# Kernel tuning notes

Measured on AMD Instinct MI355X. Metric: run time of the kernel, lower is better.

The kernel has to match this reference:

```python
import jax, jax.numpy as jnp
import numpy as np

B = 128          # graphs
NPG = 512        # nodes per graph
N = B * NPG      # total nodes
DEG = 8
E = N * DEG      # total edges (intra-graph)
D = 100          # num_feature_dim / num_node_labels
HID = 128        # config.hidden
HEADS = 8
F1 = 20          # per-head dim of first GATConv in each GATNet
RATIO = 0.5
K = int(np.ceil(RATIO * NPG))  # nodes kept per graph by SAGPooling
NEG_SLOPE = 0.2


def setup_inputs() -> dict:
    key = jax.random.key(0)
    ks = jax.random.split(key, 24)
    x = jax.random.randint(ks[0], (N,), 0, D)
    # intra-graph random edges: local ids in [0, NPG) + graph offset
    src_l = jax.random.randint(ks[1], (B, NPG * DEG), 0, NPG)
    dst_l = jax.random.randint(ks[2], (B, NPG * DEG), 0, NPG)
    off = (jnp.arange(B) * NPG)[:, None]
    edge_index = jnp.stack([(src_l + off).ravel(), (dst_l + off).ravel()])
    batch = jnp.repeat(jnp.arange(B), NPG)

    def lin(k, fan_in, fan_out):
        return jax.random.normal(k, (fan_in, fan_out), jnp.float32) / np.sqrt(fan_in)

    def att(k, h, f):
        return jax.random.normal(k, (h, f), jnp.float32) * 0.1

    p = {
        # GATNet A (conv1): GATConv(D, 20, heads=8) then GATConv(160, HID, heads=1)
        "W_a1": lin(ks[3], D, HEADS * F1), "asrc_a1": att(ks[4], HEADS, F1),
        "adst_a1": att(ks[5], HEADS, F1), "b_a1": jnp.zeros((HEADS * F1,), jnp.float32),
        "W_a2": lin(ks[6], HEADS * F1, HID), "asrc_a2": att(ks[7], 1, HID),
        "adst_a2": att(ks[8], 1, HID), "b_a2": jnp.zeros((HID,), jnp.float32),
        # GATNet B (conv4): GATConv(HID, 20, heads=8) then GATConv(160, HID, heads=1)
        "W_b1": lin(ks[9], HID, HEADS * F1), "asrc_b1": att(ks[10], HEADS, F1),
        "adst_b1": att(ks[11], HEADS, F1), "b_b1": jnp.zeros((HEADS * F1,), jnp.float32),
        "W_b2": lin(ks[12], HEADS * F1, HID), "asrc_b2": att(ks[13], 1, HID),
        "adst_b2": att(ks[14], 1, HID), "b_b2": jnp.zeros((HID,), jnp.float32),
        # SAGPooling GraphConv(HID, 1)
        "w_rel": lin(ks[15], HID, 1), "w_root": lin(ks[16], HID, 1),
        "b_pool": jnp.zeros((1,), jnp.float32),
    }
    return {"x": x, "edge_index": edge_index, "batch": batch, **p}


def _gat_conv(h, src, dst, W, asrc, adst, b):
    """PyG GATConv (with self-loops already included in src/dst)."""
    Hh, Ff = asrc.shape
    z = (h @ W).reshape(N, Hh, Ff)                       # [N,H,F]
    es = jnp.sum(z * asrc, axis=-1)                      # [N,H] source logits
    ed = jnp.sum(z * adst, axis=-1)                      # [N,H] dest logits
    e = jax.nn.leaky_relu(es[src] + ed[dst], NEG_SLOPE)  # [E',H]
    m = jax.ops.segment_max(e, dst, num_segments=N)
    m = jnp.where(jnp.isfinite(m), m, 0.0)
    ex = jnp.exp(e - m[dst])
    den = jax.ops.segment_sum(ex, dst, num_segments=N)
    alpha = ex / (den[dst] + 1e-16)
    out = jax.ops.segment_sum(z[src] * alpha[:, :, None], dst, num_segments=N)
    return out.reshape(N, Hh * Ff) + b


def reference(x, edge_index, batch,
              W_a1, asrc_a1, adst_a1, b_a1, W_a2, asrc_a2, adst_a2, b_a2,
              W_b1, asrc_b1, adst_b1, b_b1, W_b2, asrc_b2, adst_b2, b_b2,
              w_rel, w_root, b_pool):
    src, dst = edge_index[0], edge_index[1]
    loops = jnp.arange(N)
    src_sl = jnp.concatenate([src, loops])  # GATConv adds self loops
    dst_sl = jnp.concatenate([dst, loops])

    h = jax.nn.one_hot(x, D, dtype=jnp.float32)
    # GATNet A: conv1 -> relu -> conv2 ; outer relu (dropout is eval no-op)
    h = jax.nn.relu(_gat_conv(h, src_sl, dst_sl, W_a1, asrc_a1, adst_a1, b_a1))
    h = _gat_conv(h, src_sl, dst_sl, W_a2, asrc_a2, adst_a2, b_a2)
    h = jax.nn.relu(h)
    # GATNet B
    h = jax.nn.relu(_gat_conv(h, src_sl, dst_sl, W_b1, asrc_b1, adst_b1, b_b1))
    h = _gat_conv(h, src_sl, dst_sl, W_b2, asrc_b2, adst_b2, b_b2)
    h = jax.nn.relu(h)

    # SAGPooling: GraphConv(HID,1) score (no self loops), tanh, per-graph top-k
    nbr = jax.ops.segment_sum(h[src], dst, num_segments=N)
    score = jnp.tanh(nbr @ w_rel + h @ w_root + b_pool).ravel()   # [N]
    sv, si = jax.lax.top_k(score.reshape(B, NPG), K)              # [B,K]
    perm = (si + (jnp.arange(B) * NPG)[:, None]).ravel()          # global node ids
    x_sel = h[perm] * sv.ravel()[:, None]                         # [B*K, HID]
    pooled = jnp.max(x_sel.reshape(B, K, HID), axis=1)            # global_max_pool
    batch_out = jnp.repeat(jnp.arange(B), K)
    return (pooled, perm, sv.ravel(), batch_out)
```

## Files before the change

### kernel.cpp

```cpp
#include <hip/hip_runtime.h>
#include <math.h>

#define N_NODES 65536
#define NPG     512
#define NGRAPH  128
#define E_EDGES 524288
#define MAXDEG  64
#define NHEADS  8
#define F1      20
#define HID     128
#define D160    160
#define KSEL    256
#define NLBL    100

#define IMG_A2_ELEMS (144*168)
#define IMG_B1_ELEMS (176*136)
#define PB_ZERO 0
#define PB_A2   64
#define PB_B1   (PB_A2 + 95)
#define PB_B2   (PB_B1 + 94)
#define PB_WA1  (PB_B2 + 95)
#define PB_EST  (PB_WA1 + 63)
#define PB_TOT  (PB_EST + 7)

typedef unsigned short ushort_t;
typedef unsigned int   uint_t;
typedef unsigned long long u64;
typedef __attribute__((ext_vector_type(8))) short short8;
typedef __attribute__((ext_vector_type(4))) float f32x4;

__device__ __forceinline__ float lrelu(float x){ return x > 0.f ? x : 0.2f*x; }
__device__ __forceinline__ ushort_t f2bf(float f){
    uint_t u = __float_as_uint(f);
    return (ushort_t)((u + 0x7FFFu + ((u >> 16) & 1u)) >> 16);
}
__device__ __forceinline__ float bf2f(ushort_t u){ return __uint_as_float(((uint_t)u) << 16); }
__device__ __forceinline__ float bflo(uint_t v){ return __uint_as_float(v << 16); }
__device__ __forceinline__ float bfhi(uint_t v){ return __uint_as_float(v & 0xFFFF0000u); }
__device__ __forceinline__ int xswz(int bid, int nblocks){
    return (bid & 7) * (nblocks >> 3) + (bid >> 3);
}
__device__ __forceinline__ float rdlanef(float v, int i){
    return __uint_as_float((uint_t)__builtin_amdgcn_readlane(__float_as_int(v), i));
}

__device__ __forceinline__ u64 comp_make(float s, int idx){
    uint_t u = __float_as_uint(s);
    u ^= (u & 0x80000000u) ? 0xFFFFFFFFu : 0x80000000u;
    return ((u64)u << 32) | (u64)(511 - idx);
}
__device__ __forceinline__ float comp_score(u64 c){
    uint_t u = (uint_t)(c >> 32);
    u ^= (u & 0x80000000u) ? 0x80000000u : 0xFFFFFFFFu;
    return __uint_as_float(u);
}
__device__ __forceinline__ int comp_idx(u64 c){ return 511 - (int)(c & 0x1FFu); }
__device__ __forceinline__ u64 shfl_xor_u64(u64 x, int m){
    uint_t lo = __shfl_xor((uint_t)x, m);
    uint_t hi = __shfl_xor((uint_t)(x >> 32), m);
    return ((u64)hi << 32) | lo;
}

__global__ void k_prep(const float* __restrict__ Wa1, const float* __restrict__ as1,
                       const float* __restrict__ ad1,
                       const float* __restrict__ Wa2, const float* __restrict__ as2,
                       const float* __restrict__ ad2,
                       const float* __restrict__ Wb1, const float* __restrict__ asb1,
                       const float* __restrict__ adb1,
                       const float* __restrict__ Wb2, const float* __restrict__ asb2,
                       const float* __restrict__ adb2,
                       int* __restrict__ deg,
                       ushort_t* __restrict__ imgA2, ushort_t* __restrict__ imgB1,
                       ushort_t* __restrict__ imgB2,
                       ushort_t* __restrict__ Wbf, float* __restrict__ esT,
                       float* __restrict__ edT){
    int bid = blockIdx.x, tid = threadIdx.x;
    if(bid < PB_A2){
        ((uint4*)deg)[(bid - PB_ZERO)*256 + tid] = (uint4){0,0,0,0};
    } else if(bid < PB_B1 || (bid >= PB_B2 && bid < PB_WA1)){
        bool isB2 = (bid >= PB_B2);
        int j = (bid - (isB2 ? PB_B2 : PB_A2))*256 + tid;
        if(j < IMG_A2_ELEMS){
            const float* W  = isB2 ? Wb2 : Wa2;
            const float* as = isB2 ? asb2 : as2;
            const float* ad = isB2 ? adb2 : ad2;
            int n = j / 168, k = j - n*168;
            float v = 0.f;
            if(k < 160){
                if(n < 128) v = W[k*128 + n];
                else if(n < 130){
                    const float* av = (n == 128) ? as : ad;
                    float s = 0.f;
                    for(int c=0; c<128; ++c) s += W[k*128 + c]*av[c];
                    v = s;
                }
            }
            (isB2 ? imgB2 : imgA2)[j] = f2bf(v);
        }
    } else if(bid < PB_B2){
        int j = (bid - PB_B1)*256 + tid;
        if(j < IMG_B1_ELEMS){
            int n = j / 136, k = j - n*136;
            float v = 0.f;
            if(k < 128){
                if(n < 160) v = Wb1[k*160 + n];
                else {
                    int j2 = n - 160, h = j2 & 7;
                    const float* av = ((j2 < 8) ? asb1 : adb1) + h*F1;
                    const float* wr = Wb1 + k*160 + h*F1;
                    float s = 0.f;
                    #pragma unroll
                    for(int f=0; f<F1; ++f) s += wr[f]*av[f];
                    v = s;
                }
            }
            imgB1[j] = f2bf(v);
        }
    } else if(bid < PB_EST){
        int j = (bid - PB_WA1)*256 + tid;
        if(j < NLBL*D160) Wbf[j] = f2bf(Wa1[j]);
    } else {
        int t = (bid - PB_EST)*256 + tid;
        if(t < NLBL*16){
            int lbl = t >> 4, j = t & 15, h = j & 7;
            const float* av = ((j < 8) ? as1 : ad1) + h*F1;
            const float* wr = Wa1 + lbl*D160 + h*F1;
            float s = 0.f;
            #pragma unroll
            for(int f=0; f<F1; ++f) s += wr[f]*av[f];
            if(j < 8) esT[lbl*8 + h] = s;
            else      edT[lbl*8 + h] = s;
        }
    }
}

__global__ void k_build_ell(const int* __restrict__ src, const int* __restrict__ dst,
                            int* __restrict__ deg, int* __restrict__ ell){
    int blk = xswz(blockIdx.x, E_EDGES/256);
    int e = blk*blockDim.x + threadIdx.x;
    int d = dst[e];
    int p = atomicAdd(&deg[d], 1);
    if(p < MAXDEG) ell[d*MAXDEG + p] = src[e];
}

__global__ __launch_bounds__(256) void k_attn8_a(const int* __restrict__ x,
        const int* __restrict__ deg, const int* __restrict__ ell,
        const ushort_t* __restrict__ Wbf, const float* __restrict__ esT,
        const float* __restrict__ edT, const float* __restrict__ bias,
        ushort_t* __restrict__ out){
    __shared__ __align__(16) ushort_t Wl[NLBL*D160];
    __shared__ float esL[NLBL*8], edL[NLBL*8];
    int tid = threadIdx.x;
    for(int i = tid; i < NLBL*D160/8; i += 256)
        ((uint4*)Wl)[i] = ((const uint4*)Wbf)[i];
    for(int i = tid; i < NLBL*8; i += 256){ esL[i] = esT[i]; edL[i] = edT[i]; }
    __syncthreads();
    int blk = xswz(blockIdx.x, N_NODES*NHEADS/256);
    int t = blk*256 + tid;
    int n = t >> 3, h = t & 7;
    int dg = deg[n]; if(dg > MAXDEG) dg = MAXDEG;
    int lbl = x[n];
    float edn = edL[lbl*8 + h];
    float wself = expf(lrelu(esL[lbl*8 + h] + edn));
    float den = wself;
    float acc[F1];
    {
        const uint_t* zn = (const uint_t*)Wl + lbl*80 + h*10;
        #pragma unroll
        for(int f=0; f<10; ++f){
            uint_t v = zn[f];
            acc[2*f]   = wself*bflo(v);
            acc[2*f+1] = wself*bfhi(v);
        }
    }
    const int* el = ell + n*MAXDEG;
    int i = 0;
    for(; i+2 <= dg; i += 2){
        int sa = el[i], sb = el[i+1];
        int la = x[sa], lb = x[sb];
        float wa = expf(lrelu(esL[la*8 + h] + edn));
        float wb = expf(lrelu(esL[lb*8 + h] + edn));
        den += wa + wb;
        const uint_t* za = (const uint_t*)Wl + la*80 + h*10;
        const uint_t* zb = (const uint_t*)Wl + lb*80 + h*10;
        #pragma unroll
        for(int f=0; f<10; ++f){
            uint_t va = za[f], vb = zb[f];
            acc[2*f]   += wa*bflo(va) + wb*bflo(vb);
            acc[2*f+1] += wa*bfhi(va) + wb*bfhi(vb);
        }
    }
    if(i < dg){
        int sa = el[i];
        int la = x[sa];
        float wa = expf(lrelu(esL[la*8 + h] + edn));
        den += wa;
        const uint_t* za = (const uint_t*)Wl + la*80 + h*10;
        #pragma unroll
        for(int f=0; f<10; ++f){
            uint_t va = za[f];
            acc[2*f]   += wa*bflo(va);
            acc[2*f+1] += wa*bfhi(va);
        }
    }
    float inv = 1.f/(den + 1e-16f);
    uint_t* o = (uint_t*)(out + (size_t)n*D160 + h*F1);
    const float* bb = bias + h*F1;
    #pragma unroll
    for(int f=0; f<10; ++f){
        float v0 = fmaxf(acc[2*f]*inv   + bb[2*f],   0.f);
        float v1 = fmaxf(acc[2*f+1]*inv + bb[2*f+1], 0.f);
        o[f] = (uint_t)f2bf(v0) | ((uint_t)f2bf(v1) << 16);
    }
}

__global__ __launch_bounds__(512) void k_attn8b(const int* __restrict__ deg,
        const int* __restrict__ ell, const ushort_t* __restrict__ z8,
        const float* __restrict__ es8, const float* __restrict__ ed8,
        const float* __restrict__ bias, ushort_t* __restrict__ out){
    __shared__ __align__(16) ushort_t zl[512*88];
    __shared__ __align__(16) float4 esl[512];
    __shared__ __align__(16) float4 edl[512];
    int tid = threadIdx.x;
    int blk = xswz(blockIdx.x, NGRAPH*2);
    int g = blk >> 1, hg = blk & 1;
    int base = g*NPG;
    for(int idx = tid; idx < 512*10; idx += 512){
        int row = idx/10, q = idx - (idx/10)*10;
        uint4 v = *(const uint4*)(z8 + (size_t)(base+row)*D160 + hg*80 + q*8);
        *(uint4*)(zl + row*88 + q*8) = v;
    }
    esl[tid] = *(const float4*)(es8 + (size_t)(base+tid)*8 + hg*4);
    edl[tid] = *(const float4*)(ed8 + (size_t)(base+tid)*8 + hg*4);
    __syncthreads();
    int n = tid;
    int dg = deg[base+n]; if(dg > MAXDEG) dg = MAXDEG;
    const int* el = ell + (size_t)(base+n)*MAXDEG;
    float4 edn = edl[n];
    float4 esn = esl[n];
    float w0 = expf(lrelu(esn.x + edn.x));
    float w1 = expf(lrelu(esn.y + edn.y));
    float w2 = expf(lrelu(esn.z + edn.z));
    float w3 = expf(lrelu(esn.w + edn.w));
    float den0 = w0, den1 = w1, den2 = w2, den3 = w3;
    float acc[80];
    #pragma unroll
    for(int q=0; q<10; ++q){
        uint4 v = *(const uint4*)(zl + n*88 + q*8);
        const uint_t* vu = (const uint_t*)&v;
        #pragma unroll
        for(int r=0; r<4; ++r){
            int ch = q*8 + r*2;
            float wA = (ch < 20) ? w0 : (ch < 40) ? w1 : (ch < 60) ? w2 : w3;
            float wB = (ch+1 < 20) ? w0 : (ch+1 < 40) ? w1 : (ch+1 < 60) ? w2 : w3;
            acc[ch]   = wA*bflo(vu[r]);
            acc[ch+1] = wB*bfhi(vu[r]);
        }
    }
    for(int i=0; i<dg; ++i){
        int s = el[i] & (NPG-1);
        float4 es_s = esl[s];
        float wa0 = expf(lrelu(es_s.x + edn.x));
        float wa1 = expf(lrelu(es_s.y + edn.y));
        float wa2 = expf(lrelu(es_s.z + edn.z));
        float wa3 = expf(lrelu(es_s.w + edn.w));
        den0 += wa0; den1 += wa1; den2 += wa2; den3 += wa3;
        #pragma unroll
        for(int q=0; q<10; ++q){
            uint4 v = *(const uint4*)(zl + s*88 + q*8);
            const uint_t* vu = (const uint_t*)&v;
            #pragma unroll
            for(int r=0; r<4; ++r){
                int ch = q*8 + r*2;
                float wA = (ch < 20) ? wa0 : (ch < 40) ? wa1 : (ch < 60) ? wa2 : wa3;
                float wB = (ch+1 < 20) ? wa0 : (ch+1 < 40) ? wa1 : (ch+1 < 60) ? wa2 : wa3;
                acc[ch]   += wA*bflo(vu[r]);
                acc[ch+1] += wB*bfhi(vu[r]);
            }
        }
    }
    float inv0 = 1.f/(den0 + 1e-16f);
    float inv1 = 1.f/(den1 + 1e-16f);
    float inv2 = 1.f/(den2 + 1e-16f);
    float inv3 = 1.f/(den3 + 1e-16f);
    const float* bb = bias + hg*80;
    uint_t* o = (uint_t*)out + (size_t)(base+n)*80 + hg*40;
    #pragma unroll
    for(int q=0; q<10; ++q){
        #pragma unroll
        for(int r=0; r<4; ++r){
            int ch = q*8 + r*2;
            float iA = (ch < 20) ? inv0 : (ch < 40) ? inv1 : (ch < 60) ? inv2 : inv3;
            float iB = (ch+1 < 20) ? inv0 : (ch+1 < 40) ? inv1 : (ch+1 < 60) ? inv2 : inv3;
            float v0 = fmaxf(acc[ch]*iA   + bb[ch],   0.f);
            float v1 = fmaxf(acc[ch+1]*iB + bb[ch+1], 0.f);
            o[q*4 + r] = (uint_t)f2bf(v0) | ((uint_t)f2bf(v1) << 16);
        }
    }
}

template<int IN, int OUTC, int OUTIMG, bool ESED8>
__global__ __launch_bounds__(256) void k_gemm2(const ushort_t* __restrict__ Wimg,
                                               const ushort_t* __restrict__ A,
                                               ushort_t* __restrict__ C,
                                               float* __restrict__ oa,
                                               float* __restrict__ ob){
    constexpr int LDW = IN + 8;
    constexpr int NT = OUTIMG/16;
    constexpr int NC = OUTC/16;
    constexpr int KS = IN/32;
    constexpr int ELEMS = OUTIMG*LDW;
    __shared__ __align__(16) ushort_t Wt[ELEMS];
    int tid = threadIdx.x;
    int blk = xswz(blockIdx.x, N_NODES/64);
    int wave = tid >> 6, lane = tid & 63;
    int col16 = lane & 15;
    int kq = (lane >> 4) * 8;
    int row = blk*64 + wave*16 + col16;
    const ushort_t* Ar = A + (size_t)row*IN + kq;
    short8 afr[KS];
    #pragma unroll
    for(int ks=0; ks<KS; ++ks)
        afr[ks] = *reinterpret_cast<const short8*>(Ar + ks*32);
    for(int i = tid; i < ELEMS/8; i += 256)
        ((uint4*)Wt)[i] = ((const uint4*)Wimg)[i];
    __syncthreads();
    f32x4 acc[NT];
    #pragma unroll
    for(int c=0;c<NT;++c) acc[c] = (f32x4){0.f,0.f,0.f,0.f};
    #pragma unroll
    for(int ks=0; ks<KS; ++ks){
        #pragma unroll
        for(int c=0;c<NT;++c){
            short8 bf = *reinterpret_cast<const short8*>(&Wt[(c*16 + col16)*LDW + ks*32 + kq]);
            acc[c] = __builtin_amdgcn_mfma_f32_16x16x32_bf16(afr[ks], bf, acc[c], 0, 0, 0);
        }
    }
    int rbase = blk*64 + wave*16 + (lane >> 4)*4;
    #pragma unroll
    for(int c=0;c<NC;++c){
        #pragma unroll
        for(int r=0;r<4;++r){
            C[(size_t)(rbase + r)*OUTC + c*16 + col16] = f2bf(acc[c][r]);
        }
    }
    if(ESED8){
        #pragma unroll
        for(int r=0;r<4;++r){
            float v = acc[NT-1][r];
            if(col16 < 8) oa[(size_t)(rbase + r)*8 + col16] = v;
            else          ob[(size_t)(rbase + r)*8 + (col16 - 8)] = v;
        }
    } else {
        if(col16 == 0){
            #pragma unroll
            for(int r=0;r<4;++r) oa[rbase + r] = acc[NT-1][r];
        }
        if(col16 == 1){
            #pragma unroll
            for(int r=0;r<4;++r) ob[rbase + r] = acc[NT-1][r];
        }
    }
}

template<typename OutT, bool DOT>
__global__ void k_attn1(const int* __restrict__ deg, const int* __restrict__ ell,
                        const ushort_t* __restrict__ Z, const float* __restrict__ es,
                        const float* __restrict__ ed, const float* __restrict__ bias,
                        OutT* __restrict__ out,
                        const float* __restrict__ wa, const float* __restrict__ wb,
                        float* __restrict__ oa, float* __restrict__ ob){
    int blk = xswz(blockIdx.x, N_NODES/4);
    int gt = blk*blockDim.x + threadIdx.x;
    int n = gt >> 6;
    int l = threadIdx.x & 63;
    int dg = deg[n]; if(dg > MAXDEG) dg = MAXDEG;
    float edn = ed[n];
    float wself = expf(lrelu(es[n] + edn));
    int s_l = 0; float w_l = 0.f;
    if(l < dg){ s_l = ell[n*MAXDEG + l]; w_l = expf(lrelu(es[s_l] + edn)); }
    float den = w_l;
    for(int o=32;o>0;o>>=1) den += __shfl_xor(den,o);
    den += wself;
    const uint_t* Zu = (const uint_t*)Z;
    uint_t zn = Zu[(size_t)n*64 + l];
    float acc0 = wself*bflo(zn);
    float acc1 = wself*bfhi(zn);
    int i = 0;
    for(; i+4 <= dg; i += 4){
        int s0 = __builtin_amdgcn_readlane(s_l, i);
        int s1 = __builtin_amdgcn_readlane(s_l, i+1);
        int s2 = __builtin_amdgcn_readlane(s_l, i+2);
        int s3 = __builtin_amdgcn_readlane(s_l, i+3);
        uint_t z0 = Zu[(size_t)s0*64 + l];
        uint_t z1 = Zu[(size_t)s1*64 + l];
        uint_t z2 = Zu[(size_t)s2*64 + l];
        uint_t z3 = Zu[(size_t)s3*64 + l];
        float w0 = rdlanef(w_l, i);
        float w1 = rdlanef(w_l, i+1);
        float w2 = rdlanef(w_l, i+2);
        float w3 = rdlanef(w_l, i+3);
        acc0 += w0*bflo(z0) + w1*bflo(z1);
        acc1 += w0*bfhi(z0) + w1*bfhi(z1);
        acc0 += w2*bflo(z2) + w3*bflo(z3);
        acc1 += w2*bfhi(z2) + w3*bfhi(z3);
    }
    for(; i < dg; ++i){
        int s0 = __builtin_amdgcn_readlane(s_l, i);
        float w0 = rdlanef(w_l, i);
        uint_t z0 = Zu[(size_t)s0*64 + l];
        acc0 += w0*bflo(z0);
        acc1 += w0*bfhi(z0);
    }
    float inv = 1.f/(den + 1e-16f);
    float2 bb = ((const float2*)bias)[l];
    float r0 = fmaxf(acc0*inv + bb.x, 0.f);
    float r1 = fmaxf(acc1*inv + bb.y, 0.f);
    if(sizeof(OutT) == 2){
        ((uint_t*)out)[(size_t)n*64 + l] = (uint_t)f2bf(r0) | ((uint_t)f2bf(r1) << 16);
    } else {
        float2 rv; rv.x = r0; rv.y = r1;
        ((float2*)out)[(size_t)n*64 + l] = rv;
    }
    if(DOT){
        float2 a2 = ((const float2*)wa)[l];
        float2 b2 = ((const float2*)wb)[l];
        float pa = r0*a2.x + r1*a2.y;
        float pb = r0*b2.x + r1*b2.y;
        for(int o=32;o>0;o>>=1){ pa += __shfl_xor(pa,o); pb += __shfl_xor(pb,o); }
        if(l==0){ oa[n] = pa; ob[n] = pb; }
    }
}

__global__ void k_score(const int* __restrict__ deg, const int* __restrict__ ell,
                        const float* __restrict__ yrel, const float* __restrict__ rroot,
                        const float* __restrict__ bpool, float* __restrict__ score){
    int blk = xswz(blockIdx.x, N_NODES/256);
    int n = blk*blockDim.x + threadIdx.x;
    int dg = deg[n]; if(dg > MAXDEG) dg = MAXDEG;
    float s = rroot[n] + bpool[0];
    const int* el = ell + n*MAXDEG;
    int i = 0;
    for(; i+4 <= dg; i += 4){
        float y0 = yrel[el[i]],   y1 = yrel[el[i+1]];
        float y2 = yrel[el[i+2]], y3 = yrel[el[i+3]];
        s += (y0 + y1) + (y2 + y3);
    }
    for(; i < dg; ++i) s += yrel[el[i]];
    score[n] = tanhf(s);
}

__global__ __launch_bounds__(512) void k_topk_pool(const float* __restrict__ score,
                                                   const ushort_t* __restrict__ H,
                                                   float* __restrict__ pooled,
                                                   float* __restrict__ perm_f,
                                                   float* __restrict__ sv,
                                                   float* __restrict__ batch_f){
    __shared__ int   sidx[KSEL];
    __shared__ float sval[KSEL];
    __shared__ float pmax[512];
    int g = xswz(blockIdx.x, NGRAPH);
    int base = g*NPG;
    int t = threadIdx.x;
    if(t < 64){
        int l = t;
        u64 v[8];
        #pragma unroll
        for(int r=0;r<8;++r){
            int i = r*64 + l;
            v[r] = comp_make(score[base + i], i);
        }
        #pragma unroll
        for(int kk=1; kk<=9; ++kk){
            int k = 1 << kk;
            #pragma unroll
            for(int jj=kk-1; jj>=0; --jj){
                int j = 1 << jj;
                if(j < 64){
                    bool lower = (l & j) == 0;
                    #pragma unroll
                    for(int r=0;r<8;++r){
                        int i = r*64 + l;
                        u64 p = shfl_xor_u64(v[r], j);
                        bool desc = (i & k) == 0;
                        u64 mx = v[r] > p ? v[r] : p;
                        u64 mn = v[r] > p ? p : v[r];
                        v[r] = (lower == desc) ? mx : mn;
                    }
                } else {
                    int jr = j >> 6;
                    #pragma unroll
                    for(int r=0;r<8;++r){
                        if((r & jr) == 0){
                            int rp = r | jr;
                            int i = r*64 + l;
                            bool desc = (i & k) == 0;
                            u64 a = v[r], b = v[rp];
                            u64 mx = a > b ? a : b;
                            u64 mn = a > b ? b : a;
                            v[r]  = desc ? mx : mn;
                            v[rp] = desc ? mn : mx;
                        }
                    }
                }
            }
        }
        #pragma unroll
        for(int r=0;r<4;++r){
            int i = r*64 + l;
            int idx = comp_idx(v[r]);
            float s = comp_score(v[r]);
            perm_f[g*KSEL + i]  = (float)(base + idx);
            sv[g*KSEL + i]      = s;
            batch_f[g*KSEL + i] = (float)g;
            sidx[i] = idx; sval[i] = s;
        }
    }
    __syncthreads();
    int c = t & 127, kc = t >> 7;
    float mx = -1e30f;
    for(int kk = kc*64; kk < kc*64 + 64; ++kk){
        mx = fmaxf(mx, bf2f(H[(size_t)(base + sidx[kk])*HID + c]) * sval[kk]);
    }
    pmax[t] = mx;
    __syncthreads();
    if(t < HID){
        pooled[g*HID + t] = fmaxf(fmaxf(pmax[t], pmax[t+128]),
                                  fmaxf(pmax[t+256], pmax[t+384]));
    }
}

extern "C" void kernel_launch(void* const* d_in, const int* in_sizes, int n_in,
                              void* d_out, int out_size, void* d_ws, size_t ws_size,
                              hipStream_t stream) {
    const int*   x       = (const int*)  d_in[0];
    const int*   eidx    = (const int*)  d_in[1];
    const float* W_a1    = (const float*)d_in[3];
    const float* asrc_a1 = (const float*)d_in[4];
    const float* adst_a1 = (const float*)d_in[5];
    const float* b_a1    = (const float*)d_in[6];
    const float* W_a2    = (const float*)d_in[7];
    const float* asrc_a2 = (const float*)d_in[8];
    const float* adst_a2 = (const float*)d_in[9];
    const float* b_a2    = (const float*)d_in[10];
    const float* W_b1    = (const float*)d_in[11];
    const float* asrc_b1 = (const float*)d_in[12];
    const float* adst_b1 = (const float*)d_in[13];
    const float* b_b1    = (const float*)d_in[14];
    const float* W_b2    = (const float*)d_in[15];
    const float* asrc_b2 = (const float*)d_in[16];
    const float* adst_b2 = (const float*)d_in[17];
    const float* b_b2    = (const float*)d_in[18];
    const float* w_rel   = (const float*)d_in[19];
    const float* w_root  = (const float*)d_in[20];
    const float* b_pool  = (const float*)d_in[21];

    const int* e_src = eidx;
    const int* e_dst = eidx + E_EDGES;

    char* ws = (char*)d_ws;
    size_t off = 0;
    auto alloc = [&](size_t bytes)->char*{
        char* p = ws + off;
        off += (bytes + 255) & ~(size_t)255;
        return p;
    };
    int*      deg    = (int*)     alloc((size_t)N_NODES*4);
    int*      ell    = (int*)     alloc((size_t)N_NODES*MAXDEG*4);
    ushort_t* z8     = (ushort_t*)alloc((size_t)N_NODES*D160*2);
    ushort_t* h8     = (ushort_t*)alloc((size_t)N_NODES*D160*2);
    ushort_t* zc     = (ushort_t*)alloc((size_t)N_NODES*HID*2);
    ushort_t* hmid   = (ushort_t*)alloc((size_t)N_NODES*HID*2);
    ushort_t* hfin   = (ushort_t*)alloc((size_t)N_NODES*HID*2);
    float*    es8    = (float*)   alloc((size_t)N_NODES*NHEADS*4);
    float*    ed8    = (float*)   alloc((size_t)N_NODES*NHEADS*4);
    float*    es1    = (float*)   alloc((size_t)N_NODES*4);
    float*    ed1    = (float*)   alloc((size_t)N_NODES*4);
    float*    yrel   = (float*)   alloc((size_t)N_NODES*4);
    float*    rroot  = (float*)   alloc((size_t)N_NODES*4);
    float*    score  = (float*)   alloc((size_t)N_NODES*4);
    ushort_t* Wbf    = (ushort_t*)alloc((size_t)NLBL*D160*2);
    float*    esT    = (float*)   alloc((size_t)NLBL*8*4);
    float*    edT    = (float*)   alloc((size_t)NLBL*8*4);
    ushort_t* imgA2  = (ushort_t*)alloc((size_t)IMG_A2_ELEMS*2);
    ushort_t* imgB1  = (ushort_t*)alloc((size_t)IMG_B1_ELEMS*2);
    ushort_t* imgB2  = (ushort_t*)alloc((size_t)IMG_A2_ELEMS*2);
    (void)ws_size; (void)n_in; (void)in_sizes; (void)out_size;

    float* out      = (float*)d_out;
    float* pooled   = out;
    float* perm_f   = out + NGRAPH*HID;
    float* sv       = perm_f + NGRAPH*KSEL;
    float* batch_f  = sv + NGRAPH*KSEL;

    k_prep<<<PB_TOT, 256, 0, stream>>>(W_a1, asrc_a1, adst_a1,
                                       W_a2, asrc_a2, adst_a2,
                                       W_b1, asrc_b1, adst_b1,
                                       W_b2, asrc_b2, adst_b2,
                                       deg, imgA2, imgB1, imgB2, Wbf, esT, edT);
    k_build_ell<<<E_EDGES/256, 256, 0, stream>>>(e_src, e_dst, deg, ell);

    k_attn8_a<<<N_NODES*NHEADS/256, 256, 0, stream>>>(x, deg, ell, Wbf, esT, edT, b_a1, h8);

    k_gemm2<D160, HID, 144, false><<<N_NODES/64, 256, 0, stream>>>(imgA2, h8, zc, es1, ed1);
    k_attn1<ushort_t, false><<<N_NODES/4, 256, 0, stream>>>(deg, ell, zc, es1, ed1, b_a2, hmid,
                                                            nullptr, nullptr, nullptr, nullptr);

    k_gemm2<HID, D160, 176, true><<<N_NODES/64, 256, 0, stream>>>(imgB1, hmid, z8, es8, ed8);
    k_attn8b<<<NGRAPH*2, 512, 0, stream>>>(deg, ell, z8, es8, ed8, b_b1, h8);

    k_gemm2<D160, HID, 144, false><<<N_NODES/64, 256, 0, stream>>>(imgB2, h8, zc, es1, ed1);
    k_attn1<ushort_t, true><<<N_NODES/4, 256, 0, stream>>>(deg, ell, zc, es1, ed1, b_b2, hfin,
                                                           w_rel, w_root, yrel, rroot);

    k_score<<<N_NODES/256, 256, 0, stream>>>(deg, ell, yrel, rroot, b_pool, score);
    k_topk_pool<<<NGRAPH, NPG, 0, stream>>>(score, hfin, pooled, perm_f, sv, batch_f);
}
```

Baseline: 226.2 us.

## Rework single-head GAT aggregation to four threads per node with vector loads

Result: no change. 226.5 us (+0.1%).

```diff
diff --git a/kernel.cpp b/kernel.cpp
--- a/kernel.cpp
+++ b/kernel.cpp
@@ -39,9 +39,6 @@
 __device__ __forceinline__ float bfhi(uint_t v){ return __uint_as_float(v & 0xFFFF0000u); }
 __device__ __forceinline__ int xswz(int bid, int nblocks){
     return (bid & 7) * (nblocks >> 3) + (bid >> 3);
-}
-__device__ __forceinline__ float rdlanef(float v, int i){
-    return __uint_as_float((uint_t)__builtin_amdgcn_readlane(__float_as_int(v), i));
 }
 
 __device__ __forceinline__ u64 comp_make(float s, int idx){
@@ -363,72 +360,105 @@
     }
 }
 
-template<typename OutT, bool DOT>
-__global__ void k_attn1(const int* __restrict__ deg, const int* __restrict__ ell,
-                        const ushort_t* __restrict__ Z, const float* __restrict__ es,
-                        const float* __restrict__ ed, const float* __restrict__ bias,
-                        OutT* __restrict__ out,
-                        const float* __restrict__ wa, const float* __restrict__ wb,
-                        float* __restrict__ oa, float* __restrict__ ob){
-    int blk = xswz(blockIdx.x, N_NODES/4);
-    int gt = blk*blockDim.x + threadIdx.x;
-    int n = gt >> 6;
-    int l = threadIdx.x & 63;
+template<bool DOT>
+__global__ void k_attn1v(const int* __restrict__ deg, const int* __restrict__ ell,
+                         const ushort_t* __restrict__ Z, const float* __restrict__ es,
+                         const float* __restrict__ ed, const float* __restrict__ bias,
+                         ushort_t* __restrict__ out,
+                         const float* __restrict__ wa, const float* __restrict__ wb,
+                         float* __restrict__ oa, float* __restrict__ ob){
+    int blk = xswz(blockIdx.x, N_NODES*4/256);
+    int t = blk*256 + threadIdx.x;
+    int n = t >> 2, qt = t & 3;
     int dg = deg[n]; if(dg > MAXDEG) dg = MAXDEG;
     float edn = ed[n];
     float wself = expf(lrelu(es[n] + edn));
-    int s_l = 0; float w_l = 0.f;
-    if(l < dg){ s_l = ell[n*MAXDEG + l]; w_l = expf(lrelu(es[s_l] + edn)); }
-    float den = w_l;
-    for(int o=32;o>0;o>>=1) den += __shfl_xor(den,o);
-    den += wself;
-    const uint_t* Zu = (const uint_t*)Z;
-    uint_t zn = Zu[(size_t)n*64 + l];
-    float acc0 = wself*bflo(zn);
-    float acc1 = wself*bfhi(zn);
+    float den = wself;
+    const uint4* Zu = (const uint4*)Z;
+    float acc[32];
+    {
+        const uint4* zr = Zu + (size_t)n*16 + qt*4;
+        uint4 vs[4];
+        #pragma unroll
+        for(int q=0;q<4;++q) vs[q] = zr[q];
+        #pragma unroll
+        for(int q=0;q<4;++q){
+            const uint_t* vu = (const uint_t*)&vs[q];
+            #pragma unroll
+            for(int r=0;r<4;++r){
+                acc[q*8+r*2]   = wself*bflo(vu[r]);
+                acc[q*8+r*2+1] = wself*bfhi(vu[r]);
+            }
+        }
+    }
+    const int* el = ell + (size_t)n*MAXDEG;
     int i = 0;
-    for(; i+4 <= dg; i += 4){
-        int s0 = __builtin_amdgcn_readlane(s_l, i);
-        int s1 = __builtin_amdgcn_readlane(s_l, i+1);
-        int s2 = __builtin_amdgcn_readlane(s_l, i+2);
-        int s3 = __builtin_amdgcn_readlane(s_l, i+3);
-        uint_t z0 = Zu[(size_t)s0*64 + l];
-        uint_t z1 = Zu[(size_t)s1*64 + l];
-        uint_t z2 = Zu[(size_t)s2*64 + l];
-        uint_t z3 = Zu[(size_t)s3*64 + l];
-        float w0 = rdlanef(w_l, i);
-        float w1 = rdlanef(w_l, i+1);
-        float w2 = rdlanef(w_l, i+2);
-        float w3 = rdlanef(w_l, i+3);
-        acc0 += w0*bflo(z0) + w1*bflo(z1);
-        acc1 += w0*bfhi(z0) + w1*bfhi(z1);
-        acc0 += w2*bflo(z2) + w3*bflo(z3);
-        acc1 += w2*bfhi(z2) + w3*bfhi(z3);
-    }
-    for(; i < dg; ++i){
-        int s0 = __builtin_amdgcn_readlane(s_l, i);
-        float w0 = rdlanef(w_l, i);
-        uint_t z0 = Zu[(size_t)s0*64 + l];
-        acc0 += w0*bflo(z0);
-        acc1 += w0*bfhi(z0);
+    for(; i+2 <= dg; i += 2){
+        int sa = el[i], sb = el[i+1];
+        float ea = es[sa], eb = es[sb];
+        const uint4* za = Zu + (size_t)sa*16 + qt*4;
+        const uint4* zb = Zu + (size_t)sb*16 + qt*4;
+        uint4 va[4], vb4[4];
+        #pragma unroll
+        for(int q=0;q<4;++q){ va[q] = za[q]; vb4[q] = zb[q]; }
+        float wA = expf(lrelu(ea + edn));
+        float wB = expf(lrelu(eb + edn));
+        den += wA + wB;
+        #pragma unroll
+        for(int q=0;q<4;++q){
+            const uint_t* au = (const uint_t*)&va[q];
+            const uint_t* bu = (const uint_t*)&vb4[q];
+            #pragma unroll
+            for(int r=0;r<4;++r){
+                acc[q*8+r*2]   += wA*bflo(au[r]) + wB*bflo(bu[r]);
+                acc[q*8+r*2+1] += wA*bfhi(au[r]) + wB*bfhi(bu[r]);
+            }
+        }
+    }
+    if(i < dg){
+        int sa = el[i];
+        float ea = es[sa];
+        const uint4* za = Zu + (size_t)sa*16 + qt*4;
+        uint4 va[4];
+        #pragma unroll
+        for(int q=0;q<4;++q) va[q] = za[q];
+        float wA = expf(lrelu(ea + edn));
+        den += wA;
+        #pragma unroll
+        for(int q=0;q<4;++q){
+            const uint_t* au = (const uint_t*)&va[q];
+            #pragma unroll
+            for(int r=0;r<4;++r){
+                acc[q*8+r*2]   += wA*bflo(au[r]);
+                acc[q*8+r*2+1] += wA*bfhi(au[r]);
+            }
+        }
     }
     float inv = 1.f/(den + 1e-16f);
-    float2 bb = ((const float2*)bias)[l];
-    float r0 = fmaxf(acc0*inv + bb.x, 0.f);
-    float r1 = fmaxf(acc1*inv + bb.y, 0.f);
-    if(sizeof(OutT) == 2){
-        ((uint_t*)out)[(size_t)n*64 + l] = (uint_t)f2bf(r0) | ((uint_t)f2bf(r1) << 16);
-    } else {
-        float2 rv; rv.x = r0; rv.y = r1;
-        ((float2*)out)[(size_t)n*64 + l] = rv;
+    const float* bb = bias + qt*32;
+    float pa = 0.f, pb = 0.f;
+    uint_t* o = (uint_t*)out + (size_t)n*64 + qt*16;
+    #pragma unroll
+    for(int q=0;q<4;++q){
+        uint4 w;
+        uint_t* wu = (uint_t*)&w;
+        #pragma unroll
+        for(int r=0;r<4;++r){
+            int ch = q*8 + r*2;
+            float r0 = fmaxf(acc[ch]*inv   + bb[ch],   0.f);
+            float r1 = fmaxf(acc[ch+1]*inv + bb[ch+1], 0.f);
+            wu[r] = (uint_t)f2bf(r0) | ((uint_t)f2bf(r1) << 16);
+            if(DOT){
+                pa += r0*wa[qt*32 + ch] + r1*wa[qt*32 + ch + 1];
+                pb += r0*wb[qt*32 + ch] + r1*wb[qt*32 + ch + 1];
+            }
+        }
+        *(uint4*)(o + q*4) = w;
     }
     if(DOT){
-        float2 a2 = ((const float2*)wa)[l];
-        float2 b2 = ((const float2*)wb)[l];
-        float pa = r0*a2.x + r1*a2.y;
-        float pb = r0*b2.x + r1*b2.y;
-        for(int o=32;o>0;o>>=1){ pa += __shfl_xor(pa,o); pb += __shfl_xor(pb,o); }
-        if(l==0){ oa[n] = pa; ob[n] = pb; }
+        pa += __shfl_xor(pa, 1); pa += __shfl_xor(pa, 2);
+        pb += __shfl_xor(pb, 1); pb += __shfl_xor(pb, 2);
+        if(qt == 0){ oa[n] = pa; ob[n] = pb; }
     }
 }
 
@@ -603,15 +633,15 @@
     k_attn8_a<<<N_NODES*NHEADS/256, 256, 0, stream>>>(x, deg, ell, Wbf, esT, edT, b_a1, h8);
 
     k_gemm2<D160, HID, 144, false><<<N_NODES/64, 256, 0, stream>>>(imgA2, h8, zc, es1, ed1);
-    k_attn1<ushort_t, false><<<N_NODES/4, 256, 0, stream>>>(deg, ell, zc, es1, ed1, b_a2, hmid,
-                                                            nullptr, nullptr, nullptr, nullptr);
+    k_attn1v<false><<<N_NODES*4/256, 256, 0, stream>>>(deg, ell, zc, es1, ed1, b_a2, hmid,
+                                                       nullptr, nullptr, nullptr, nullptr);
 
     k_gemm2<HID, D160, 176, true><<<N_NODES/64, 256, 0, stream>>>(imgB1, hmid, z8, es8, ed8);
     k_attn8b<<<NGRAPH*2, 512, 0, stream>>>(deg, ell, z8, es8, ed8, b_b1, h8);
 
     k_gemm2<D160, HID, 144, false><<<N_NODES/64, 256, 0, stream>>>(imgB2, h8, zc, es1, ed1);
-    k_attn1<ushort_t, true><<<N_NODES/4, 256, 0, stream>>>(deg, ell, zc, es1, ed1, b_b2, hfin,
-                                                           w_rel, w_root, yrel, rroot);
+    k_attn1v<true><<<N_NODES*4/256, 256, 0, stream>>>(deg, ell, zc, es1, ed1, b_b2, hfin,
+                                                      w_rel, w_root, yrel, rroot);
 
     k_score<<<N_NODES/256, 256, 0, stream>>>(deg, ell, yrel, rroot, b_pool, score);
     k_topk_pool<<<NGRAPH, NPG, 0, stream>>>(score, hfin, pooled, perm_f, sv, batch_f);
```
